# Performance work log

Hardware: AMD Instinct MI355X
Metric: run time of the kernel (lower is better)

## Reference

```python
import jax, jax.numpy as jnp
import numpy as np

H = 1024      # hidden_size
NH = 16       # num heads
HD = H // NH  # head dim


def setup_inputs() -> dict:
    key = jax.random.key(0)
    ks = jax.random.split(key, 10)
    B, S = 2, 2048
    bound = 1.0 / np.sqrt(H)
    def w(k):
        return jax.random.uniform(k, (H, H), jnp.float32, -bound, bound)
    def b(k):
        return jax.random.uniform(k, (H,), jnp.float32, -bound, bound)
    return {
        "hidden_states": jax.random.normal(ks[0], (B, S, H), jnp.float32),
        "attention_mask": jnp.zeros((B, 1, 1, S), jnp.float32),
        "wq": w(ks[1]), "bq": b(ks[2]),
        "wk": w(ks[3]), "bk": b(ks[4]),
        "wv": w(ks[5]), "bv": b(ks[6]),
        "wo": w(ks[7]), "bo": b(ks[8]),
    }


def reference(hidden_states, attention_mask, wq, bq, wk, bk, wv, bv, wo, bo):
    B, S, _ = hidden_states.shape
    # linear layers: y = x @ W^T + b (torch F.linear convention)
    q = hidden_states @ wq.T + bq
    k = hidden_states @ wk.T + bk
    v = hidden_states @ wv.T + bv
    # [B, NH, S, HD]
    q = q.reshape(B, S, NH, HD).transpose(0, 2, 1, 3)
    k = k.reshape(B, S, NH, HD).transpose(0, 2, 1, 3)
    v = v.reshape(B, S, NH, HD).transpose(0, 2, 1, 3)
    scores = jnp.einsum("bhqd,bhkd->bhqk", q, k) / jnp.sqrt(jnp.float32(HD))
    scores = scores + attention_mask
    probs = jax.nn.softmax(scores, axis=-1)  # dropout_p=0 -> no dropout
    ctx = jnp.einsum("bhqk,bhkd->bhqd", probs, v)
    ctx = ctx.transpose(0, 2, 1, 3).reshape(B, S, H)
    return ctx @ wo.T + bo
```

## Files before the change

### kernel.cpp

```cpp
#include <hip/hip_runtime.h>
#include <hip/hip_bf16.h>

typedef unsigned short u16;
typedef __attribute__((ext_vector_type(4))) float f32x4;
typedef __attribute__((ext_vector_type(8))) __bf16 bf16x8;

#define NH 16
#define HD 64
#define HID 1024
#define SS 2048
#define MM 4096

__device__ __forceinline__ u16 f2b(float f) {
  unsigned u = __builtin_bit_cast(unsigned, f);
  u += 0x7fff + ((u >> 16) & 1);
  return (u16)(u >> 16);
}

__device__ __forceinline__ float fexp2(float x) {
#if __has_builtin(__builtin_amdgcn_exp2f)
  return __builtin_amdgcn_exp2f(x);
#else
  return exp2f(x);
#endif
}

template <int CTRL>
__device__ __forceinline__ float dpp_mv(float x) {
  int xi = __builtin_bit_cast(int, x);
  int yi = __builtin_amdgcn_update_dpp(xi, xi, CTRL, 0xF, 0xF, true);
  return __builtin_bit_cast(float, yi);
}
__device__ __forceinline__ float dppmax16(float v) {
  v = fmaxf(v, dpp_mv<0xB1>(v));
  v = fmaxf(v, dpp_mv<0x4E>(v));
  v = fmaxf(v, dpp_mv<0x141>(v));
  v = fmaxf(v, dpp_mv<0x140>(v));
  return v;
}
__device__ __forceinline__ float dppsum16(float v) {
  v += dpp_mv<0xB1>(v);
  v += dpp_mv<0x4E>(v);
  v += dpp_mv<0x141>(v);
  v += dpp_mv<0x140>(v);
  return v;
}

__device__ __forceinline__ void gl_lds16(const u16* g, u16* l) {
  __builtin_amdgcn_global_load_lds(
      (const __attribute__((address_space(1))) void*)g,
      (__attribute__((address_space(3))) void*)l, 16, 0, 0);
}

__global__ void cvt4(const float* __restrict__ src, u16* __restrict__ dst, int n4) {
  int i = blockIdx.x * 256 + threadIdx.x;
  if (i >= n4) return;
  float4 v = reinterpret_cast<const float4*>(src)[i];
  ushort4 o;
  o.x = f2b(v.x); o.y = f2b(v.y); o.z = f2b(v.z); o.w = f2b(v.w);
  reinterpret_cast<ushort4*>(dst)[i] = o;
}

__global__ void cvt4w(const float* __restrict__ s0, const float* __restrict__ s1,
                      const float* __restrict__ s2, const float* __restrict__ s3,
                      u16* __restrict__ d0, u16* __restrict__ d1,
                      u16* __restrict__ d2, u16* __restrict__ d3) {
  const int w = blockIdx.y;
  const float* src = (w == 0) ? s0 : (w == 1) ? s1 : (w == 2) ? s2 : s3;
  u16* dst = (w == 0) ? d0 : (w == 1) ? d1 : (w == 2) ? d2 : d3;
  int i = blockIdx.x * 256 + threadIdx.x;
  float4 v = reinterpret_cast<const float4*>(src)[i];
  ushort4 o;
  o.x = f2b(v.x); o.y = f2b(v.y); o.z = f2b(v.z); o.w = f2b(v.w);
  reinterpret_cast<ushort4*>(dst)[i] = o;
}

__global__ __launch_bounds__(256)
void gemm_qkv(const u16* __restrict__ xb,
              const u16* __restrict__ wqb, const u16* __restrict__ wkb, const u16* __restrict__ wvb,
              const float* __restrict__ bq, const float* __restrict__ bk, const float* __restrict__ bv,
              u16* __restrict__ qh, u16* __restrict__ kh, u16* __restrict__ vt) {
  const int mt = blockIdx.x;
  const int nt = blockIdx.y;
  const int wi = nt >> 3;
  const int n0 = (nt & 7) << 7;
  const int m0 = mt << 7;
  const u16* wb = (wi == 0) ? wqb : (wi == 1) ? wkb : wvb;
  const float* bias = (wi == 0) ? bq : (wi == 1) ? bk : bv;

  __shared__ u16 at[128 * 64];
  __shared__ u16 bt[128 * 64];

  const int tid = threadIdx.x;
  const int wave = tid >> 6;
  const int lane = tid & 63;
  const int g = lane >> 4;
  const int wm = (wave >> 1) << 6;
  const int wn = (wave & 1) << 6;
  const int lr = lane & 15;
  const int rb = g << 2;
  const int lrow = lane >> 3;
  const int dslot = lane & 7;

  f32x4 acc[4][4] = {};

  for (int k0 = 0; k0 < HID; k0 += 64) {
    __syncthreads();
    #pragma unroll
    for (int i = 0; i < 4; i++) {
      const int row = wave * 32 + i * 8 + lrow;
      const int scol = (dslot ^ (row & 7)) << 3;
      gl_lds16(&xb[(size_t)(m0 + row) * HID + k0 + scol], at + wave * 2048 + i * 512);
      gl_lds16(&wb[(size_t)(n0 + row) * HID + k0 + scol], bt + wave * 2048 + i * 512);
    }
    __syncthreads();
    #pragma unroll
    for (int kk = 0; kk < 2; kk++) {
      bf16x8 af[4], bfr[4];
      #pragma unroll
      for (int i = 0; i < 4; i++) {
        const int ra = wm + i * 16 + lr;
        const int rbw = wn + i * 16 + lr;
        const int sa_ = ((kk << 2) + g) ^ (ra & 7);
        const int sb_ = ((kk << 2) + g) ^ (rbw & 7);
        af[i]  = *reinterpret_cast<const bf16x8*>(&at[ra * 64 + (sa_ << 3)]);
        bfr[i] = *reinterpret_cast<const bf16x8*>(&bt[rbw * 64 + (sb_ << 3)]);
      }
      #pragma unroll
      for (int i = 0; i < 4; i++)
        #pragma unroll
        for (int j = 0; j < 4; j++)
          acc[i][j] = __builtin_amdgcn_mfma_f32_16x16x32_bf16(af[i], bfr[j], acc[i][j], 0, 0, 0);
    }
  }

  #pragma unroll
  for (int i = 0; i < 4; i++) {
    #pragma unroll
    for (int j = 0; j < 4; j++) {
      #pragma unroll
      for (int r = 0; r < 4; r++) {
        const int m = m0 + wm + i * 16 + rb + r;
        const int n = n0 + wn + j * 16 + lr;
        const float val = acc[i][j][r] + bias[n];
        const u16 bv16 = f2b(val);
        const int b = m >> 11, s = m & 2047;
        const int h = n >> 6, d = n & 63;
        if (wi == 0)      qh[((size_t)(b * NH + h) * SS + s) * HD + d] = bv16;
        else if (wi == 1) kh[((size_t)(b * NH + h) * SS + s) * HD + d] = bv16;
        else              vt[((size_t)(b * NH + h) * HD + d) * SS + s] = bv16;
      }
    }
  }
}

__global__ __launch_bounds__(256, 2)
void attn(const u16* __restrict__ qh, const u16* __restrict__ kh, const u16* __restrict__ vt,
          const float* __restrict__ mask, u16* __restrict__ ctxb) {
  const int id = blockIdx.x;
  const int bh = (id & 7) + 8 * ((id >> 3) & 3);
  const int qt = id >> 5;
  const int b = bh >> 4;
  const int h = bh & 15;
  const int q0 = qt << 7;

  const int tid = threadIdx.x;
  const int wave = tid >> 6;
  const int lane = tid & 63;
  const int g = lane >> 4;
  const int lr = lane & 15;
  const int lk = g << 3;
  const int rb = g << 2;
  const int lrow = lane >> 3;
  const int dslot = lane & 7;

  const u16* qb = qh + (size_t)bh * SS * HD;
  const u16* kb = kh + (size_t)bh * SS * HD;
  const u16* vb = vt + (size_t)bh * HD * SS;
  const float* mrow = mask + (size_t)b * SS;

  __shared__ u16 kt[2][64 * 64];
  __shared__ u16 vtile[2][64 * 64];
  __shared__ u16 pt[4][32][72];

  const int qrow0 = q0 + wave * 32;

  bf16x8 qf[2][2];
  #pragma unroll
  for (int c = 0; c < 2; c++)
    #pragma unroll
    for (int dk = 0; dk < 2; dk++)
      qf[c][dk] = *reinterpret_cast<const bf16x8*>(
          &qb[(size_t)(qrow0 + c * 16 + lr) * HD + dk * 32 + lk]);

  f32x4 o[2][4] = {};
  float mrun[2][4], lrun[2][4];
  #pragma unroll
  for (int c = 0; c < 2; c++)
    #pragma unroll
    for (int r = 0; r < 4; r++) { mrun[c][r] = -1e30f; lrun[c][r] = 0.f; }

  const float LOG2E = 1.4426950408889634f;
  const float SCL = 0.125f * LOG2E;

  auto stage = [&](u16* kdst, u16* vdst, int kv0) {
    #pragma unroll
    for (int i = 0; i < 2; i++) {
      const int row = wave * 16 + i * 8 + lrow;
      const int scol = (dslot ^ (row & 7)) << 3;
      gl_lds16(&kb[(size_t)(kv0 + row) * HD + scol], kdst + wave * 1024 + i * 512);
      gl_lds16(&vb[(size_t)row * SS + kv0 + scol], vdst + wave * 1024 + i * 512);
    }
  };

  stage(kt[0], vtile[0], 0);
  __syncthreads();

  for (int it = 0; it < SS / 64; ++it) {
    const int cur = it & 1;
    if (it + 1 < SS / 64)
      stage(kt[cur ^ 1], vtile[cur ^ 1], (it + 1) * 64);

    const int kv0 = it * 64;
    const u16* kc = kt[cur];
    const u16* vc = vtile[cur];

    f32x4 sa[2][4] = {};
    #pragma unroll
    for (int ks = 0; ks < 4; ks++) {
      const int row = ks * 16 + lr;
      const int s0 = g ^ (row & 7);
      const int s1 = (g + 4) ^ (row & 7);
      const bf16x8 kf0 = *reinterpret_cast<const bf16x8*>(&kc[row * 64 + (s0 << 3)]);
      const bf16x8 kf1 = *reinterpret_cast<const bf16x8*>(&kc[row * 64 + (s1 << 3)]);
      #pragma unroll
      for (int c = 0; c < 2; c++) {
        sa[c][ks] = __builtin_amdgcn_mfma_f32_16x16x32_bf16(qf[c][0], kf0, sa[c][ks], 0, 0, 0);
        sa[c][ks] = __builtin_amdgcn_mfma_f32_16x16x32_bf16(qf[c][1], kf1, sa[c][ks], 0, 0, 0);
      }
    }

    float mk2[4];
    #pragma unroll
    for (int ks = 0; ks < 4; ks++) mk2[ks] = mrow[kv0 + ks * 16 + lr] * LOG2E;

    float tmax[2][4];
    #pragma unroll
    for (int c = 0; c < 2; c++) {
      #pragma unroll
      for (int r = 0; r < 4; r++) tmax[c][r] = -1e30f;
      #pragma unroll
      for (int ks = 0; ks < 4; ks++)
        #pragma unroll
        for (int r = 0; r < 4; r++) {
          const float v = fmaf(sa[c][ks][r], SCL, mk2[ks]);
          sa[c][ks][r] = v;
          tmax[c][r] = fmaxf(tmax[c][r], v);
        }
    }

    float need = -1e30f;
    #pragma unroll
    for (int c = 0; c < 2; c++)
      #pragma unroll
      for (int r = 0; r < 4; r++) need = fmaxf(need, tmax[c][r] - mrun[c][r]);
    if (!__all(need <= 4.0f)) {
      #pragma unroll
      for (int c = 0; c < 2; c++)
        #pragma unroll
        for (int r = 0; r < 4; r++) {
          const float rowmax = dppmax16(tmax[c][r]);
          const float mnew = fmaxf(mrun[c][r], rowmax);
          const float alpha = fexp2(mrun[c][r] - mnew);
          mrun[c][r] = mnew;
          lrun[c][r] *= alpha;
          #pragma unroll
          for (int ds = 0; ds < 4; ds++) o[c][ds][r] *= alpha;
        }
    }

    #pragma unroll
    for (int c = 0; c < 2; c++)
      #pragma unroll
      for (int ks = 0; ks < 4; ks++)
        #pragma unroll
        for (int r = 0; r < 4; r++) {
          const float p = fexp2(sa[c][ks][r] - mrun[c][r]);
          lrun[c][r] += p;
          pt[wave][c * 16 + rb + r][ks * 16 + lr] = f2b(p);
        }

    bf16x8 pa[2][2];
    #pragma unroll
    for (int c = 0; c < 2; c++)
      #pragma unroll
      for (int ko = 0; ko < 2; ko++)
        pa[c][ko] = *reinterpret_cast<const bf16x8*>(&pt[wave][c * 16 + lr][ko * 32 + lk]);

    #pragma unroll
    for (int ds = 0; ds < 4; ds++) {
      #pragma unroll
      for (int ko = 0; ko < 2; ko++) {
        const int vrow = ds * 16 + lr;
        const int vs = ((ko << 2) + g) ^ (vrow & 7);
        const bf16x8 vf = *reinterpret_cast<const bf16x8*>(&vc[vrow * 64 + (vs << 3)]);
        #pragma unroll
        for (int c = 0; c < 2; c++)
          o[c][ds] = __builtin_amdgcn_mfma_f32_16x16x32_bf16(pa[c][ko], vf, o[c][ds], 0, 0, 0);
      }
    }
    __syncthreads();
  }

  #pragma unroll
  for (int c = 0; c < 2; c++) {
    float inv[4];
    #pragma unroll
    for (int r = 0; r < 4; r++) inv[r] = 1.0f / dppsum16(lrun[c][r]);
    #pragma unroll
    for (int ds = 0; ds < 4; ds++)
      #pragma unroll
      for (int r = 0; r < 4; r++) {
        const int srow = qrow0 + c * 16 + rb + r;
        ctxb[(size_t)(b * SS + srow) * HID + h * HD + ds * 16 + lr] = f2b(o[c][ds][r] * inv[r]);
      }
  }
}

__global__ __launch_bounds__(256)
void gemm_out(const u16* __restrict__ ab, const u16* __restrict__ wb,
              const float* __restrict__ bias, float* __restrict__ out) {
  const int m0 = blockIdx.x << 7;
  const int n0 = blockIdx.y << 6;

  __shared__ u16 at[128 * 64];
  __shared__ u16 bt[64 * 64];

  const int tid = threadIdx.x;
  const int wave = tid >> 6;
  const int lane = tid & 63;
  const int g = lane >> 4;
  const int wm = wave << 5;
  const int lr = lane & 15;
  const int rb = g << 2;
  const int lrow = lane >> 3;
  const int dslot = lane & 7;

  f32x4 acc[2][4] = {};

  for (int k0 = 0; k0 < HID; k0 += 64) {
    __syncthreads();
    #pragma unroll
    for (int i = 0; i < 4; i++) {
      const int row = wave * 32 + i * 8 + lrow;
      const int scol = (dslot ^ (row & 7)) << 3;
      gl_lds16(&ab[(size_t)(m0 + row) * HID + k0 + scol], at + wave * 2048 + i * 512);
    }
    #pragma unroll
    for (int i = 0; i < 2; i++) {
      const int row = wave * 16 + i * 8 + lrow;
      const int scol = (dslot ^ (row & 7)) << 3;
      gl_lds16(&wb[(size_t)(n0 + row) * HID + k0 + scol], bt + wave * 1024 + i * 512);
    }
    __syncthreads();
    #pragma unroll
    for (int kk = 0; kk < 2; kk++) {
      bf16x8 af[2], bfr[4];
      #pragma unroll
      for (int i = 0; i < 2; i++) {
        const int ra = wm + i * 16 + lr;
        const int sa_ = ((kk << 2) + g) ^ (ra & 7);
        af[i] = *reinterpret_cast<const bf16x8*>(&at[ra * 64 + (sa_ << 3)]);
      }
      #pragma unroll
      for (int j = 0; j < 4; j++) {
        const int rbw = j * 16 + lr;
        const int sb_ = ((kk << 2) + g) ^ (rbw & 7);
        bfr[j] = *reinterpret_cast<const bf16x8*>(&bt[rbw * 64 + (sb_ << 3)]);
      }
      #pragma unroll
      for (int i = 0; i < 2; i++)
        #pragma unroll
        for (int j = 0; j < 4; j++)
          acc[i][j] = __builtin_amdgcn_mfma_f32_16x16x32_bf16(af[i], bfr[j], acc[i][j], 0, 0, 0);
    }
  }

  #pragma unroll
  for (int i = 0; i < 2; i++)
    #pragma unroll
    for (int j = 0; j < 4; j++)
      #pragma unroll
      for (int r = 0; r < 4; r++) {
        const int m = m0 + wm + i * 16 + rb + r;
        const int n = n0 + j * 16 + lr;
        out[(size_t)m * HID + n] = acc[i][j][r] + bias[n];
      }
}

extern "C" void kernel_launch(void* const* d_in, const int* in_sizes, int n_in,
                              void* d_out, int out_size, void* d_ws, size_t ws_size,
                              hipStream_t stream) {
  const float* hs   = (const float*)d_in[0];
  const float* mask = (const float*)d_in[1];
  const float* wq   = (const float*)d_in[2];
  const float* bq   = (const float*)d_in[3];
  const float* wk   = (const float*)d_in[4];
  const float* bk   = (const float*)d_in[5];
  const float* wv   = (const float*)d_in[6];
  const float* bv   = (const float*)d_in[7];
  const float* wo   = (const float*)d_in[8];
  const float* bo   = (const float*)d_in[9];
  float* out = (float*)d_out;

  char* ws = (char*)d_ws;
  u16* xb   = (u16*)(ws);
  u16* ctxb = (u16*)(ws + ((size_t)8  << 20));
  u16* qhb  = (u16*)(ws + ((size_t)16 << 20));
  u16* khb  = (u16*)(ws + ((size_t)24 << 20));
  u16* vtb  = (u16*)(ws + ((size_t)32 << 20));
  u16* wqb  = (u16*)(ws + ((size_t)40 << 20));
  u16* wkb  = (u16*)(ws + ((size_t)42 << 20));
  u16* wvb  = (u16*)(ws + ((size_t)44 << 20));
  u16* wob  = (u16*)(ws + ((size_t)46 << 20));

  cvt4<<<4096, 256, 0, stream>>>(hs, xb, MM * HID / 4);
  cvt4w<<<dim3(1024, 4), 256, 0, stream>>>(wq, wk, wv, wo, wqb, wkb, wvb, wob);

  gemm_qkv<<<dim3(32, 24), 256, 0, stream>>>(xb, wqb, wkb, wvb, bq, bk, bv, qhb, khb, vtb);
  attn<<<512, 256, 0, stream>>>(qhb, khb, vtb, mask, ctxb);
  gemm_out<<<dim3(32, 16), 256, 0, stream>>>(ctxb, wob, bo, out);
}
```

Baseline: 144.7 us.

## Compute transposed S=K·Q^T so each lane owns a query row for softmax

Swaps the MFMA operand order in the QK^T step so the score accumulator is transposed: each lane holds four keys of a single query row instead of one key across four rows. The row max and row sum then need only two cross-lane xor shuffles rather than four DPP steps for each of eight rows. Running max/sum state shrinks to two scalars per lane, the mask is read as a float4, and P is written to LDS as packed 8-byte stores with a wider padded row. The rescale path now broadcasts alpha with shuffles back to the output accumulator layout, which adds some cross-lane traffic when rescaling happens.

```diff
diff --git a/kernel.cpp b/kernel.cpp
--- a/kernel.cpp
+++ b/kernel.cpp
@@ -23,27 +23,6 @@
 #else
   return exp2f(x);
 #endif
-}
-
-template <int CTRL>
-__device__ __forceinline__ float dpp_mv(float x) {
-  int xi = __builtin_bit_cast(int, x);
-  int yi = __builtin_amdgcn_update_dpp(xi, xi, CTRL, 0xF, 0xF, true);
-  return __builtin_bit_cast(float, yi);
-}
-__device__ __forceinline__ float dppmax16(float v) {
-  v = fmaxf(v, dpp_mv<0xB1>(v));
-  v = fmaxf(v, dpp_mv<0x4E>(v));
-  v = fmaxf(v, dpp_mv<0x141>(v));
-  v = fmaxf(v, dpp_mv<0x140>(v));
-  return v;
-}
-__device__ __forceinline__ float dppsum16(float v) {
-  v += dpp_mv<0xB1>(v);
-  v += dpp_mv<0x4E>(v);
-  v += dpp_mv<0x141>(v);
-  v += dpp_mv<0x140>(v);
-  return v;
 }
 
 __device__ __forceinline__ void gl_lds16(const u16* g, u16* l) {
@@ -181,7 +160,7 @@
 
   __shared__ u16 kt[2][64 * 64];
   __shared__ u16 vtile[2][64 * 64];
-  __shared__ u16 pt[4][32][72];
+  __shared__ __align__(16) u16 pt[4][32][80];
 
   const int qrow0 = q0 + wave * 32;
 
@@ -194,11 +173,8 @@
           &qb[(size_t)(qrow0 + c * 16 + lr) * HD + dk * 32 + lk]);
 
   f32x4 o[2][4] = {};
-  float mrun[2][4], lrun[2][4];
-  #pragma unroll
-  for (int c = 0; c < 2; c++)
-    #pragma unroll
-    for (int r = 0; r < 4; r++) { mrun[c][r] = -1e30f; lrun[c][r] = 0.f; }
+  float mrun[2] = {-1e30f, -1e30f};
+  float lrun[2] = {0.f, 0.f};
 
   const float LOG2E = 1.4426950408889634f;
   const float SCL = 0.125f * LOG2E;
@@ -235,60 +211,62 @@
       const bf16x8 kf1 = *reinterpret_cast<const bf16x8*>(&kc[row * 64 + (s1 << 3)]);
       #pragma unroll
       for (int c = 0; c < 2; c++) {
-        sa[c][ks] = __builtin_amdgcn_mfma_f32_16x16x32_bf16(qf[c][0], kf0, sa[c][ks], 0, 0, 0);
-        sa[c][ks] = __builtin_amdgcn_mfma_f32_16x16x32_bf16(qf[c][1], kf1, sa[c][ks], 0, 0, 0);
-      }
-    }
-
-    float mk2[4];
-    #pragma unroll
-    for (int ks = 0; ks < 4; ks++) mk2[ks] = mrow[kv0 + ks * 16 + lr] * LOG2E;
-
-    float tmax[2][4];
-    #pragma unroll
-    for (int c = 0; c < 2; c++) {
-      #pragma unroll
-      for (int r = 0; r < 4; r++) tmax[c][r] = -1e30f;
+        sa[c][ks] = __builtin_amdgcn_mfma_f32_16x16x32_bf16(kf0, qf[c][0], sa[c][ks], 0, 0, 0);
+        sa[c][ks] = __builtin_amdgcn_mfma_f32_16x16x32_bf16(kf1, qf[c][1], sa[c][ks], 0, 0, 0);
+      }
+    }
+
+    f32x4 mk4[4];
+    #pragma unroll
+    for (int ks = 0; ks < 4; ks++)
+      mk4[ks] = *reinterpret_cast<const f32x4*>(&mrow[kv0 + ks * 16 + rb]);
+
+    float tmax[2] = {-1e30f, -1e30f};
+    #pragma unroll
+    for (int c = 0; c < 2; c++)
       #pragma unroll
       for (int ks = 0; ks < 4; ks++)
         #pragma unroll
         for (int r = 0; r < 4; r++) {
-          const float v = fmaf(sa[c][ks][r], SCL, mk2[ks]);
+          const float v = fmaf(sa[c][ks][r], SCL, mk4[ks][r] * LOG2E);
           sa[c][ks][r] = v;
-          tmax[c][r] = fmaxf(tmax[c][r], v);
+          tmax[c] = fmaxf(tmax[c], v);
         }
-    }
-
-    float need = -1e30f;
-    #pragma unroll
-    for (int c = 0; c < 2; c++)
-      #pragma unroll
-      for (int r = 0; r < 4; r++) need = fmaxf(need, tmax[c][r] - mrun[c][r]);
+
+    const float need = fmaxf(tmax[0] - mrun[0], tmax[1] - mrun[1]);
     if (!__all(need <= 4.0f)) {
       #pragma unroll
-      for (int c = 0; c < 2; c++)
+      for (int c = 0; c < 2; c++) {
+        float rm = tmax[c];
+        rm = fmaxf(rm, __shfl_xor(rm, 16));
+        rm = fmaxf(rm, __shfl_xor(rm, 32));
+        const float mnew = fmaxf(mrun[c], rm);
+        const float alpha = fexp2(mrun[c] - mnew);
+        mrun[c] = mnew;
+        lrun[c] *= alpha;
         #pragma unroll
         for (int r = 0; r < 4; r++) {
-          const float rowmax = dppmax16(tmax[c][r]);
-          const float mnew = fmaxf(mrun[c][r], rowmax);
-          const float alpha = fexp2(mrun[c][r] - mnew);
-          mrun[c][r] = mnew;
-          lrun[c][r] *= alpha;
+          const float ar = __shfl(alpha, (lane & 48) | (rb + r));
           #pragma unroll
-          for (int ds = 0; ds < 4; ds++) o[c][ds][r] *= alpha;
+          for (int ds = 0; ds < 4; ds++) o[c][ds][r] *= ar;
         }
+      }
     }
 
     #pragma unroll
     for (int c = 0; c < 2; c++)
       #pragma unroll
-      for (int ks = 0; ks < 4; ks++)
-        #pragma unroll
-        for (int r = 0; r < 4; r++) {
-          const float p = fexp2(sa[c][ks][r] - mrun[c][r]);
-          lrun[c][r] += p;
-          pt[wave][c * 16 + rb + r][ks * 16 + lr] = f2b(p);
-        }
+      for (int ks = 0; ks < 4; ks++) {
+        const float p0 = fexp2(sa[c][ks][0] - mrun[c]);
+        const float p1 = fexp2(sa[c][ks][1] - mrun[c]);
+        const float p2 = fexp2(sa[c][ks][2] - mrun[c]);
+        const float p3 = fexp2(sa[c][ks][3] - mrun[c]);
+        lrun[c] += (p0 + p1) + (p2 + p3);
+        uint2 w;
+        w.x = (unsigned)f2b(p0) | ((unsigned)f2b(p1) << 16);
+        w.y = (unsigned)f2b(p2) | ((unsigned)f2b(p3) << 16);
+        *reinterpret_cast<uint2*>(&pt[wave][c * 16 + lr][ks * 16 + rb]) = w;
+      }
 
     bf16x8 pa[2][2];
     #pragma unroll
@@ -314,9 +292,14 @@
 
   #pragma unroll
   for (int c = 0; c < 2; c++) {
+    float lt = lrun[c];
+    lt += __shfl_xor(lt, 16);
+    lt += __shfl_xor(lt, 32);
+    const float invl = 1.0f / lt;
     float inv[4];
     #pragma unroll
-    for (int r = 0; r < 4; r++) inv[r] = 1.0f / dppsum16(lrun[c][r]);
+    for (int r = 0; r < 4; r++)
+      inv[r] = __shfl(invl, (lane & 48) | (rb + r));
     #pragma unroll
     for (int ds = 0; ds < 4; ds++)
       #pragma unroll
```

New measurement: 153.1 us. 5.8% more time.

## Triple-buffer attention K/V tiles with vmcnt waits and merge conversion kernels

Applied to the files above, without the earlier changes.

The attention kernel moves from double to triple buffering of K/V LDS tiles. Each thread waits only on its oldest loads with s_waitcnt vmcnt, then a single barrier replaces the end-of-iteration __syncthreads, so the prefetch runs two tiles ahead. Separately, the activation and weight fp32-to-bf16 conversions are merged into one launch to remove a kernel launch. The changes raise LDS use per block, which may lower occupancy, and rely on the hand-counted vmcnt being correct.

```diff
diff --git a/kernel.cpp b/kernel.cpp
--- a/kernel.cpp
+++ b/kernel.cpp
@@ -52,27 +52,26 @@
       (__attribute__((address_space(3))) void*)l, 16, 0, 0);
 }
 
-__global__ void cvt4(const float* __restrict__ src, u16* __restrict__ dst, int n4) {
-  int i = blockIdx.x * 256 + threadIdx.x;
-  if (i >= n4) return;
-  float4 v = reinterpret_cast<const float4*>(src)[i];
+__global__ void cvt_all(const float* __restrict__ hs,
+                        const float* __restrict__ wq, const float* __restrict__ wk,
+                        const float* __restrict__ wv, const float* __restrict__ wo,
+                        u16* __restrict__ xb, u16* __restrict__ wqb,
+                        u16* __restrict__ wkb, u16* __restrict__ wvb,
+                        u16* __restrict__ wob) {
+  const int i = blockIdx.x * 256 + threadIdx.x;
+  const float* src; u16* dst; int off;
+  if (i < 1048576) { src = hs; dst = xb; off = i; }
+  else {
+    const int j = i - 1048576;
+    const int w = j >> 18;
+    off = j & 262143;
+    src = (w == 0) ? wq : (w == 1) ? wk : (w == 2) ? wv : wo;
+    dst = (w == 0) ? wqb : (w == 1) ? wkb : (w == 2) ? wvb : wob;
+  }
+  float4 v = reinterpret_cast<const float4*>(src)[off];
   ushort4 o;
   o.x = f2b(v.x); o.y = f2b(v.y); o.z = f2b(v.z); o.w = f2b(v.w);
-  reinterpret_cast<ushort4*>(dst)[i] = o;
-}
-
-__global__ void cvt4w(const float* __restrict__ s0, const float* __restrict__ s1,
-                      const float* __restrict__ s2, const float* __restrict__ s3,
-                      u16* __restrict__ d0, u16* __restrict__ d1,
-                      u16* __restrict__ d2, u16* __restrict__ d3) {
-  const int w = blockIdx.y;
-  const float* src = (w == 0) ? s0 : (w == 1) ? s1 : (w == 2) ? s2 : s3;
-  u16* dst = (w == 0) ? d0 : (w == 1) ? d1 : (w == 2) ? d2 : d3;
-  int i = blockIdx.x * 256 + threadIdx.x;
-  float4 v = reinterpret_cast<const float4*>(src)[i];
-  ushort4 o;
-  o.x = f2b(v.x); o.y = f2b(v.y); o.z = f2b(v.z); o.w = f2b(v.w);
-  reinterpret_cast<ushort4*>(dst)[i] = o;
+  reinterpret_cast<ushort4*>(dst)[off] = o;
 }
 
 __global__ __launch_bounds__(256)
@@ -179,8 +178,8 @@
   const u16* vb = vt + (size_t)bh * HD * SS;
   const float* mrow = mask + (size_t)b * SS;
 
-  __shared__ u16 kt[2][64 * 64];
-  __shared__ u16 vtile[2][64 * 64];
+  __shared__ u16 kt[3][64 * 64];
+  __shared__ u16 vtile[3][64 * 64];
   __shared__ u16 pt[4][32][72];
 
   const int qrow0 = q0 + wave * 32;
@@ -214,12 +213,18 @@
   };
 
   stage(kt[0], vtile[0], 0);
-  __syncthreads();
+  stage(kt[1], vtile[1], 64);
 
   for (int it = 0; it < SS / 64; ++it) {
-    const int cur = it & 1;
-    if (it + 1 < SS / 64)
-      stage(kt[cur ^ 1], vtile[cur ^ 1], (it + 1) * 64);
+    if (it < SS / 64 - 1) asm volatile("s_waitcnt vmcnt(4)" ::: "memory");
+    else                  asm volatile("s_waitcnt vmcnt(0)" ::: "memory");
+    __builtin_amdgcn_s_barrier();
+
+    const int cur = it % 3;
+    if (it + 2 < SS / 64) {
+      const int nxt = (it + 2) % 3;
+      stage(kt[nxt], vtile[nxt], (it + 2) * 64);
+    }
 
     const int kv0 = it * 64;
     const u16* kc = kt[cur];
@@ -309,7 +314,6 @@
           o[c][ds] = __builtin_amdgcn_mfma_f32_16x16x32_bf16(pa[c][ko], vf, o[c][ds], 0, 0, 0);
       }
     }
-    __syncthreads();
   }
 
   #pragma unroll
@@ -424,8 +428,7 @@
   u16* wvb  = (u16*)(ws + ((size_t)44 << 20));
   u16* wob  = (u16*)(ws + ((size_t)46 << 20));
 
-  cvt4<<<4096, 256, 0, stream>>>(hs, xb, MM * HID / 4);
-  cvt4w<<<dim3(1024, 4), 256, 0, stream>>>(wq, wk, wv, wo, wqb, wkb, wvb, wob);
+  cvt_all<<<8192, 256, 0, stream>>>(hs, wq, wk, wv, wo, xb, wqb, wkb, wvb, wob);
 
   gemm_qkv<<<dim3(32, 24), 256, 0, stream>>>(xb, wqb, wkb, wvb, bq, bk, bv, qhb, khb, vtb);
   attn<<<512, 256, 0, stream>>>(qhb, khb, vtb, mask, ctxb);
```

Result: faster. 140.6 us, median of 2 (-2.8%).
